# Kernel optimization log

Hardware: AMD Instinct MI355X
Metric: run time of the kernel (lower is better)

## Reference

```python
import jax, jax.numpy as jnp
import numpy as np

RADIUS = 1.5
PARTITION_NUM = 5
OUT_CHANNEL = 128
IN_CHANNEL = 64
EPS = 1e-5


def setup_inputs() -> dict:
    key = jax.random.key(0)
    ks = jax.random.split(key, 10)
    B, N, npoint, K = 16, 8192, 2048, 32
    D = 61  # points feature dim; in_channel = D + 3 = 64
    xyz = jax.random.normal(ks[0], (B, N, 3), dtype=jnp.float32)
    points = jax.random.normal(ks[1], (B, N, D), dtype=jnp.float32)
    local_coordinates = jax.random.uniform(ks[2], (B, npoint, K, 3), dtype=jnp.float32)
    neighbor_lists = jax.random.randint(ks[3], (B, npoint, K), 0, N)
    data_idx = jax.random.randint(ks[4], (B, npoint), 0, N)
    parameter_list = jnp.zeros((1,), dtype=jnp.float32)
    # params (torch Linear stored transposed here: [in, out])
    W1 = jax.random.normal(ks[5], (IN_CHANNEL * PARTITION_NUM, OUT_CHANNEL), dtype=jnp.float32) * 0.02
    b1 = jnp.zeros((OUT_CHANNEL,), dtype=jnp.float32)
    g1 = jnp.ones((OUT_CHANNEL,), dtype=jnp.float32)
    be1 = jnp.zeros((OUT_CHANNEL,), dtype=jnp.float32)
    W2 = jax.random.normal(ks[6], (OUT_CHANNEL, OUT_CHANNEL), dtype=jnp.float32) * 0.02
    b2 = jnp.zeros((OUT_CHANNEL,), dtype=jnp.float32)
    g2 = jnp.ones((OUT_CHANNEL,), dtype=jnp.float32)
    be2 = jnp.zeros((OUT_CHANNEL,), dtype=jnp.float32)
    return dict(xyz=xyz, points=points, local_coordinates=local_coordinates,
                neighbor_lists=neighbor_lists, parameter_list=parameter_list,
                data_idx=data_idx, W1=W1, b1=b1, g1=g1, be1=be1,
                W2=W2, b2=b2, g2=g2, be2=be2)


def _forward(xyz, points, local_coordinates, parameter_list,
             W1, b1, g1, be1, W2, b2, g2, be2, neighbor_lists, data_idx):
    B, N, _ = xyz.shape
    _, npoint, K = neighbor_lists.shape
    # new_xyz = index_points(xyz, data_idx)
    new_xyz = jnp.take_along_axis(xyz, data_idx[:, :, None], axis=1)  # [B, npoint, 3]
    # points = cat(points, xyz) -> in_channel features
    pts = jnp.concatenate([points, xyz], axis=2)  # [B, N, C]
    C = pts.shape[-1]
    # gather neighbor feats: [B, npoint, K, C] (permute chain in torch is a net identity)
    idx = neighbor_lists.reshape(B, npoint * K)
    grouped = jnp.take_along_axis(pts, idx[:, :, None], axis=1).reshape(B, npoint, K, C)
    # circle_conv: radial binning + scatter-add over partition bins
    lc = local_coordinates.reshape(B, npoint, K, 3)
    dist = jnp.linalg.norm(lc[..., 0:2], axis=-1)          # [B, npoint, K]
    dist = jnp.minimum(dist / RADIUS, 0.99)                # cut(x, 0.99)
    bins = jnp.floor(dist * PARTITION_NUM).astype(jnp.int32)
    onehot = jax.nn.one_hot(bins, PARTITION_NUM, dtype=grouped.dtype)  # [B, npoint, K, P]
    feature = jnp.einsum('bnkp,bnkc->bnpc', onehot, grouped)           # scatter_add
    feature = feature.reshape(B * npoint, PARTITION_NUM * C)
    # Linear + BatchNorm1d (training-mode batch stats) + ReLU
    x = feature @ W1 + b1                                  # [B*npoint, out]
    mu = x.mean(axis=0)
    var = x.var(axis=0)
    x = jax.nn.relu(g1 * (x - mu) / jnp.sqrt(var + EPS) + be1)
    x = x.reshape(B, npoint, -1)
    # Linear + BatchNorm1d over channels + ReLU
    y = x @ W2 + b2                                        # [B, npoint, out]
    mu2 = y.mean(axis=(0, 1))
    var2 = y.var(axis=(0, 1))
    new_points = jax.nn.relu(g2 * (y - mu2) / jnp.sqrt(var2 + EPS) + be2)
    return new_xyz, new_points


def reference(xyz, points, local_coordinates, neighbor_lists, parameter_list,
              data_idx, W1, b1, g1, be1, W2, b2, g2, be2):
    return _forward(xyz, points, local_coordinates, parameter_list,
                    W1, b1, g1, be1, W2, b2, g2, be2, neighbor_lists, data_idx)
```

## Files before the change

### kernel.cpp

```cpp
#include <hip/hip_runtime.h>
#include <hip/hip_bf16.h>
#include <math.h>

#define B_SZ     16
#define N_PTS    8192
#define NPOINT   2048
#define KNBR     32
#define D_FEAT   61
#define C_IN     64
#define P_BINS   5
#define C_OUT    128
#define M_ROWS   (B_SZ * NPOINT)
#define K1       (C_IN * P_BINS)
#define EPSV     1e-5f

typedef __attribute__((ext_vector_type(8))) short bf16x8;
typedef __attribute__((ext_vector_type(4))) float f32x4;

__device__ __forceinline__ unsigned short f2bf_rne(float v) {
    unsigned u = __float_as_uint(v);
    u += 0x7fffu + ((u >> 16) & 1u);
    return (unsigned short)(u >> 16);
}
__device__ __forceinline__ float bf2f(unsigned short v) {
    return __uint_as_float(((unsigned)v) << 16);
}

__device__ __forceinline__ size_t fragB_idx(int n, int c) {
    return ((size_t)((c >> 5) * 8 + (n >> 4)) << 9) +
           ((((c >> 3) & 3) * 16 + (n & 15)) << 3) + (c & 7);
}

__global__ __launch_bounds__(256) void prep_kernel(
    const float* __restrict__ W1, const float* __restrict__ W2,
    unsigned short* __restrict__ W1f, unsigned short* __restrict__ W2f,
    float* __restrict__ st)
{
    const int gid = blockIdx.x * 256 + threadIdx.x;
    if (gid < 40960) {
        int c = gid >> 7, n = gid & 127;
        W1f[fragB_idx(n, c)] = f2bf_rne(W1[gid]);
    } else if (gid < 57344) {
        int i = gid - 40960;
        int c = i >> 7, n = i & 127;
        W2f[fragB_idx(n, c)] = f2bf_rne(W2[i]);
    } else if (gid < 61440) {
        st[gid - 57344] = 0.f;
    }
}

__global__ __launch_bounds__(256) void fusedg1_kernel(
    const float* __restrict__ xyz, const float* __restrict__ points,
    const float* __restrict__ lc, const int* __restrict__ nl,
    const int* __restrict__ didx, const unsigned short* __restrict__ W1f,
    const float* __restrict__ b1, unsigned short* __restrict__ x1f,
    float* __restrict__ st, float* __restrict__ newxyz)
{
    const int g    = blockIdx.x;
    const int xcd  = g & 7;
    const int slot = g >> 3;
    const int b    = 2 * xcd + (slot >> 7);
    const int t16  = slot & 127;
    const int tile = b * 128 + t16;
    const int wave = threadIdx.x >> 6;
    const int lane = threadIdx.x & 63;
    const int k    = lane & 31;
    const int lm   = lane & 15, kg = lane >> 4;
    const int kgl  = (lane >> 3) & 3, jl = lane & 7, khalf = lane >> 5;

    __shared__ int s_srt[4][32];
    __shared__ __align__(16) unsigned short sA[10 * 512];

    const float* __restrict__ pbase = points + (size_t)b * N_PTS * D_FEAT;
    const float* __restrict__ xbase = xyz + (size_t)b * N_PTS * 3;

    for (int p = 0; p < 4; ++p) {
        const int mloc = wave * 4 + p;
        const int bid  = tile * 16 + mloc;
        const size_t nbase = (size_t)bid * KNBR;

        const float x = lc[(nbase + k) * 3 + 0];
        const float y = lc[(nbase + k) * 3 + 1];
        const float dd = fminf(sqrtf(x * x + y * y) * (1.0f / 1.5f), 0.99f);
        int bin = (int)(dd * 5.0f);
        bin = bin > 4 ? 4 : (bin < 0 ? 0 : bin);
        const int n = nl[nbase + k];

        unsigned m0 = (unsigned)__ballot(bin == 0);
        unsigned m1 = (unsigned)__ballot(bin == 1);
        unsigned m2 = (unsigned)__ballot(bin == 2);
        unsigned m3 = (unsigned)__ballot(bin == 3);
        unsigned m4 = (unsigned)__ballot(bin == 4);
        const int c0n = __popc(m0), c1n = __popc(m1);
        const int c2n = __popc(m2), c3n = __popc(m3);
        const int e0 = c0n, e1 = e0 + c1n, e2 = e1 + c2n, e3 = e2 + c3n;

        int start = (bin > 0 ? c0n : 0) + (bin > 1 ? c1n : 0) +
                    (bin > 2 ? c2n : 0) + (bin > 3 ? c3n : 0);
        unsigned mymask = m0;
        mymask = bin == 1 ? m1 : mymask;
        mymask = bin == 2 ? m2 : mymask;
        mymask = bin == 3 ? m3 : mymask;
        mymask = bin == 4 ? m4 : mymask;
        const int pos = start + __popc(mymask & ((1u << k) - 1u));

        if (lane < 32) s_srt[wave][pos] = n;
        if (lane >= 32 && lane < 35) {
            const int di = didx[bid];
            newxyz[(size_t)bid * 3 + (lane - 32)] = xbase[(size_t)di * 3 + (lane - 32)];
        }

        float v[32];
        #pragma unroll
        for (int kk = 0; kk < 32; ++kk) {
            const int nr = __builtin_amdgcn_readfirstlane(s_srt[wave][kk]);
            float t;
            if (lane < D_FEAT) t = pbase[nr * D_FEAT + lane];
            else               t = xbase[nr * 3 + (lane - D_FEAT)];
            v[kk] = t;
        }

        float acc = 0.f, pre0 = 0.f, pre1 = 0.f, pre2 = 0.f, pre3 = 0.f;
        #pragma unroll
        for (int kk = 0; kk < 32; ++kk) {
            acc += v[kk];
            const int kp = kk + 1;
            if (kp == e0) pre0 = acc;
            if (kp == e1) pre1 = acc;
            if (kp == e2) pre2 = acc;
            if (kp == e3) pre3 = acc;
        }
        float vals[5];
        vals[0] = pre0;
        vals[1] = pre1 - pre0;
        vals[2] = pre2 - pre1;
        vals[3] = pre3 - pre2;
        vals[4] = acc - pre3;

        #pragma unroll
        for (int bb = 0; bb < 5; ++bb) {
            const int kb = bb * 2 + khalf;
            sA[kb * 512 + (kgl * 16 + mloc) * 8 + jl] = f2bf_rne(vals[bb]);
        }
    }
    __syncthreads();

    f32x4 acc0 = {}, acc1 = {};
    #pragma unroll
    for (int kb = 0; kb < 10; ++kb) {
        bf16x8 a = *(const bf16x8*)&sA[kb * 512 + lane * 8];
        bf16x8 w0 = *(const bf16x8*)(W1f + ((size_t)(kb * 8 + wave * 2) << 9) + lane * 8);
        bf16x8 w1 = *(const bf16x8*)(W1f + ((size_t)(kb * 8 + wave * 2 + 1) << 9) + lane * 8);
        acc0 = __builtin_amdgcn_mfma_f32_16x16x32_bf16(a, w0, acc0, 0, 0, 0);
        acc1 = __builtin_amdgcn_mfma_f32_16x16x32_bf16(a, w1, acc1, 0, 0, 0);
    }

    const int rep = (g & 7) * 128;
    #pragma unroll
    for (int q = 0; q < 2; ++q) {
        const f32x4 A = q ? acc1 : acc0;
        const int col = (wave * 2 + q) * 16 + lm;
        const float bb = b1[col];
        float ls = 0.f, lq = 0.f;
        #pragma unroll
        for (int i = 0; i < 4; ++i) {
            float vv = A[i] + bb;
            const size_t idx = (((size_t)(tile * 4 + (col >> 5))) << 9) +
                               ((((col >> 3) & 3) * 16 + kg * 4 + i) << 3) + (col & 7);
            x1f[idx] = f2bf_rne(vv);
            ls += vv; lq += vv * vv;
        }
        ls += __shfl_xor(ls, 16); ls += __shfl_xor(ls, 32);
        lq += __shfl_xor(lq, 16); lq += __shfl_xor(lq, 32);
        if (kg == 0) {
            atomicAdd(&st[rep + col], ls);
            atomicAdd(&st[1024 + rep + col], lq);
        }
    }
}

__global__ __launch_bounds__(256) void gemm2_mfma(
    const unsigned short* __restrict__ Xf,
    const float* __restrict__ st_in,
    const float* __restrict__ g1, const float* __restrict__ be1,
    const unsigned short* __restrict__ Wf, const float* __restrict__ bias,
    unsigned short* __restrict__ out, float* __restrict__ st)
{
    __shared__ float sc[128], sh[128];
    __shared__ float s_s[4][128], s_q[4][128];
    const int tid = threadIdx.x;
    if (tid < 128) {
        float s = 0.f, q = 0.f;
        #pragma unroll
        for (int r = 0; r < 8; ++r) {
            s += st_in[r * 128 + tid];
            q += st_in[1024 + r * 128 + tid];
        }
        float mu  = s * (1.0f / (float)M_ROWS);
        float var = q * (1.0f / (float)M_ROWS) - mu * mu;
        float iv  = 1.0f / sqrtf(var + EPSV);
        float sg  = g1[tid] * iv;
        sc[tid] = sg;
        sh[tid] = be1[tid] - mu * sg;
    }
    __syncthreads();

    const int g    = blockIdx.x;
    const int xcd  = g & 7;
    const int slot = g >> 3;
    const int bb_  = 2 * xcd + (slot >> 5);
    const int tile = (bb_ * 32 + (slot & 31)) * 4 + (tid >> 6);

    const int wave = tid >> 6, lane = tid & 63;
    const int lm = lane & 15, kg = lane >> 4;

    f32x4 acc[8] = {};
    #pragma unroll
    for (int kb = 0; kb < 4; ++kb) {
        const int c0 = kb * 32 + kg * 8;
        bf16x8 xr = *(const bf16x8*)(Xf + (((size_t)(tile * 4 + kb)) << 9) + lane * 8);
        f32x4 s0 = *(const f32x4*)&sc[c0];
        f32x4 s1 = *(const f32x4*)&sc[c0 + 4];
        f32x4 h0 = *(const f32x4*)&sh[c0];
        f32x4 h1 = *(const f32x4*)&sh[c0 + 4];
        bf16x8 a;
        #pragma unroll
        for (int j = 0; j < 4; ++j) {
            a[j]     = (short)f2bf_rne(fmaxf(0.f, s0[j] * bf2f((unsigned short)xr[j]) + h0[j]));
            a[4 + j] = (short)f2bf_rne(fmaxf(0.f, s1[j] * bf2f((unsigned short)xr[4 + j]) + h1[j]));
        }
        #pragma unroll
        for (int nf = 0; nf < 8; ++nf) {
            bf16x8 bfr = *(const bf16x8*)(Wf + (((size_t)(kb * 8 + nf)) << 9) + lane * 8);
            acc[nf] = __builtin_amdgcn_mfma_f32_16x16x32_bf16(a, bfr, acc[nf], 0, 0, 0);
        }
    }

    const int orow = tile * 16 + kg * 4;
    #pragma unroll
    for (int nf = 0; nf < 8; ++nf) {
        const int col = nf * 16 + lm;
        const float bb = bias[col];
        float ls = 0.f, lq = 0.f;
        #pragma unroll
        for (int i = 0; i < 4; ++i) {
            float v = acc[nf][i] + bb;
            out[(size_t)(orow + i) * C_OUT + col] = f2bf_rne(v);
            ls += v; lq += v * v;
        }
        ls += __shfl_xor(ls, 16); ls += __shfl_xor(ls, 32);
        lq += __shfl_xor(lq, 16); lq += __shfl_xor(lq, 32);
        if (kg == 0) { s_s[wave][col] = ls; s_q[wave][col] = lq; }
    }
    __syncthreads();
    if (tid < 128) {
        const int rep = (g & 7) * 128;
        float ts = s_s[0][tid] + s_s[1][tid] + s_s[2][tid] + s_s[3][tid];
        float tq = s_q[0][tid] + s_q[1][tid] + s_q[2][tid] + s_q[3][tid];
        atomicAdd(&st[2048 + rep + tid], ts);
        atomicAdd(&st[3072 + rep + tid], tq);
    }
}

__global__ __launch_bounds__(256) void out_kernel(
    const unsigned short* __restrict__ Y, const float* __restrict__ st,
    const float* __restrict__ g2, const float* __restrict__ be2,
    float* __restrict__ out)
{
    __shared__ float sc[128], sh[128];
    const int tid = threadIdx.x;
    if (tid < 128) {
        float s = 0.f, q = 0.f;
        #pragma unroll
        for (int r = 0; r < 8; ++r) {
            s += st[2048 + r * 128 + tid];
            q += st[3072 + r * 128 + tid];
        }
        float mu  = s * (1.0f / (float)M_ROWS);
        float var = q * (1.0f / (float)M_ROWS) - mu * mu;
        float iv  = 1.0f / sqrtf(var + EPSV);
        float sg  = g2[tid] * iv;
        sc[tid] = sg;
        sh[tid] = be2[tid] - mu * sg;
    }
    __syncthreads();

    const size_t e8 = (size_t)blockIdx.x * 256 + tid;
    bf16x8 v = ((const bf16x8*)Y)[e8];
    const int cb = (int)((e8 * 8) & 127);
    float4 r0, r1;
    r0.x = fmaxf(0.f, sc[cb + 0] * bf2f((unsigned short)v[0]) + sh[cb + 0]);
    r0.y = fmaxf(0.f, sc[cb + 1] * bf2f((unsigned short)v[1]) + sh[cb + 1]);
    r0.z = fmaxf(0.f, sc[cb + 2] * bf2f((unsigned short)v[2]) + sh[cb + 2]);
    r0.w = fmaxf(0.f, sc[cb + 3] * bf2f((unsigned short)v[3]) + sh[cb + 3]);
    r1.x = fmaxf(0.f, sc[cb + 4] * bf2f((unsigned short)v[4]) + sh[cb + 4]);
    r1.y = fmaxf(0.f, sc[cb + 5] * bf2f((unsigned short)v[5]) + sh[cb + 5]);
    r1.z = fmaxf(0.f, sc[cb + 6] * bf2f((unsigned short)v[6]) + sh[cb + 6]);
    r1.w = fmaxf(0.f, sc[cb + 7] * bf2f((unsigned short)v[7]) + sh[cb + 7]);
    ((float4*)out)[e8 * 2]     = r0;
    ((float4*)out)[e8 * 2 + 1] = r1;
}

extern "C" void kernel_launch(void* const* d_in, const int* in_sizes, int n_in,
                              void* d_out, int out_size, void* d_ws, size_t ws_size,
                              hipStream_t stream)
{
    const float* xyz    = (const float*)d_in[0];
    const float* points = (const float*)d_in[1];
    const float* lc     = (const float*)d_in[2];
    const int*   nl     = (const int*)d_in[3];
    const int*   didx   = (const int*)d_in[5];
    const float* W1     = (const float*)d_in[6];
    const float* b1     = (const float*)d_in[7];
    const float* g1     = (const float*)d_in[8];
    const float* be1    = (const float*)d_in[9];
    const float* W2     = (const float*)d_in[10];
    const float* b2     = (const float*)d_in[11];
    const float* g2     = (const float*)d_in[12];
    const float* be2    = (const float*)d_in[13];

    float* out = (float*)d_out;
    char*  ws  = (char*)d_ws;

    unsigned short* x1f = (unsigned short*)ws;
    unsigned short* yb  = (unsigned short*)(ws + 8388608);
    unsigned short* W1f = (unsigned short*)(ws + 16777216);
    unsigned short* W2f = (unsigned short*)(ws + 16859136);
    float*          st  = (float*)(ws + 16891904);

    prep_kernel<<<240, 256, 0, stream>>>(W1, W2, W1f, W2f, st);
    fusedg1_kernel<<<M_ROWS / 16, 256, 0, stream>>>(xyz, points, lc, nl, didx,
                                                    W1f, b1, x1f, st, out);
    gemm2_mfma<<<M_ROWS / 64, 256, 0, stream>>>(x1f, st, g1, be1,
                                                W2f, b2, yb, st);
    out_kernel<<<(M_ROWS * C_OUT) / (256 * 8), 256, 0, stream>>>(
        yb, st, g2, be2, out + (size_t)M_ROWS * 3);
}
```

Measured before the change: 168.4 us.

## Pre-pack point features to bf16 rows and retile gemm2 with wider stat replicas

A new prep pass converts points+xyz into a padded bf16 [B*N,64] table, so the neighbor gather in the fused first GEMM reads aligned 128-byte rows instead of fp32 61-wide rows plus a separate xyz lookup. Binning is done as direct per-bin accumulation rather than prefix sums. gemm2 switches to 16-row tiles with column-split waves and more blocks, and the BatchNorm statistic replicas grow from 8 to 16 to reduce atomic contention. The extra conversion pass reads and writes the full point table, which adds memory traffic, and bf16 inputs reduce precision before summation.

```diff
diff --git a/kernel.cpp b/kernel.cpp
--- a/kernel.cpp
+++ b/kernel.cpp
@@ -13,6 +13,7 @@
 #define M_ROWS   (B_SZ * NPOINT)
 #define K1       (C_IN * P_BINS)
 #define EPSV     1e-5f
+#define NREP     16
 
 typedef __attribute__((ext_vector_type(8))) short bf16x8;
 typedef __attribute__((ext_vector_type(4))) float f32x4;
@@ -32,25 +33,41 @@
 }
 
 __global__ __launch_bounds__(256) void prep_kernel(
+    const float* __restrict__ points, const float* __restrict__ xyz,
     const float* __restrict__ W1, const float* __restrict__ W2,
-    unsigned short* __restrict__ W1f, unsigned short* __restrict__ W2f,
-    float* __restrict__ st)
-{
-    const int gid = blockIdx.x * 256 + threadIdx.x;
-    if (gid < 40960) {
-        int c = gid >> 7, n = gid & 127;
-        W1f[fragB_idx(n, c)] = f2bf_rne(W1[gid]);
-    } else if (gid < 57344) {
-        int i = gid - 40960;
-        int c = i >> 7, n = i & 127;
-        W2f[fragB_idx(n, c)] = f2bf_rne(W2[i]);
-    } else if (gid < 61440) {
-        st[gid - 57344] = 0.f;
+    unsigned short* __restrict__ ptsb, unsigned short* __restrict__ W1f,
+    unsigned short* __restrict__ W2f, float* __restrict__ st)
+{
+    const int blk = blockIdx.x;
+    const int tid = threadIdx.x;
+    if (blk < 32768) {
+        const int xcd  = blk & 7;
+        const int slot = blk >> 3;
+        const int b    = 2 * xcd + (slot >> 11);
+        const int rin  = (slot & 2047) * 4 + (tid >> 6);
+        const int row  = b * N_PTS + rin;
+        const int c    = tid & 63;
+        float v;
+        if (c < D_FEAT) v = points[(size_t)row * D_FEAT + c];
+        else            v = xyz[(size_t)row * 3 + (c - D_FEAT)];
+        ptsb[((size_t)row << 6) | c] = f2bf_rne(v);
+    } else {
+        const int gid = (blk - 32768) * 256 + tid;
+        if (gid < 40960) {
+            int c = gid >> 7, n = gid & 127;
+            W1f[fragB_idx(n, c)] = f2bf_rne(W1[gid]);
+        } else if (gid < 57344) {
+            int i = gid - 40960;
+            int c = i >> 7, n = i & 127;
+            W2f[fragB_idx(n, c)] = f2bf_rne(W2[i]);
+        } else {
+            st[gid - 57344] = 0.f;
+        }
     }
 }
 
 __global__ __launch_bounds__(256) void fusedg1_kernel(
-    const float* __restrict__ xyz, const float* __restrict__ points,
+    const unsigned short* __restrict__ ptsb, const float* __restrict__ xyz,
     const float* __restrict__ lc, const int* __restrict__ nl,
     const int* __restrict__ didx, const unsigned short* __restrict__ W1f,
     const float* __restrict__ b1, unsigned short* __restrict__ x1f,
@@ -60,8 +77,7 @@
     const int xcd  = g & 7;
     const int slot = g >> 3;
     const int b    = 2 * xcd + (slot >> 7);
-    const int t16  = slot & 127;
-    const int tile = b * 128 + t16;
+    const int tile = b * 128 + (slot & 127);
     const int wave = threadIdx.x >> 6;
     const int lane = threadIdx.x & 63;
     const int k    = lane & 31;
@@ -71,7 +87,7 @@
     __shared__ int s_srt[4][32];
     __shared__ __align__(16) unsigned short sA[10 * 512];
 
-    const float* __restrict__ pbase = points + (size_t)b * N_PTS * D_FEAT;
+    const unsigned short* __restrict__ tb = ptsb + (((size_t)b * N_PTS) << 6);
     const float* __restrict__ xbase = xyz + (size_t)b * N_PTS * 3;
 
     for (int p = 0; p < 4; ++p) {
@@ -110,33 +126,27 @@
             newxyz[(size_t)bid * 3 + (lane - 32)] = xbase[(size_t)di * 3 + (lane - 32)];
         }
 
-        float v[32];
+        const int srtv = s_srt[wave][k];
+
+        unsigned short vv[32];
         #pragma unroll
         for (int kk = 0; kk < 32; ++kk) {
-            const int nr = __builtin_amdgcn_readfirstlane(s_srt[wave][kk]);
-            float t;
-            if (lane < D_FEAT) t = pbase[nr * D_FEAT + lane];
-            else               t = xbase[nr * 3 + (lane - D_FEAT)];
-            v[kk] = t;
-        }
-
-        float acc = 0.f, pre0 = 0.f, pre1 = 0.f, pre2 = 0.f, pre3 = 0.f;
+            const int nr = __builtin_amdgcn_readlane(srtv, kk);
+            vv[kk] = tb[((size_t)nr << 6) | lane];
+        }
+
+        float a0 = 0.f, a1 = 0.f, a2 = 0.f, a3 = 0.f, a4 = 0.f;
         #pragma unroll
         for (int kk = 0; kk < 32; ++kk) {
-            acc += v[kk];
-            const int kp = kk + 1;
-            if (kp == e0) pre0 = acc;
-            if (kp == e1) pre1 = acc;
-            if (kp == e2) pre2 = acc;
-            if (kp == e3) pre3 = acc;
-        }
-        float vals[5];
-        vals[0] = pre0;
-        vals[1] = pre1 - pre0;
-        vals[2] = pre2 - pre1;
-        vals[3] = pre3 - pre2;
-        vals[4] = acc - pre3;
-
+            const float v = bf2f(vv[kk]);
+            if      (kk < e0) a0 += v;
+            else if (kk < e1) a1 += v;
+            else if (kk < e2) a2 += v;
+            else if (kk < e3) a3 += v;
+            else              a4 += v;
+        }
+
+        const float vals[5] = {a0, a1, a2, a3, a4};
         #pragma unroll
         for (int bb = 0; bb < 5; ++bb) {
             const int kb = bb * 2 + khalf;
@@ -155,7 +165,7 @@
         acc1 = __builtin_amdgcn_mfma_f32_16x16x32_bf16(a, w1, acc1, 0, 0, 0);
     }
 
-    const int rep = (g & 7) * 128;
+    const int rep = (g & (NREP - 1)) * 128;
     #pragma unroll
     for (int q = 0; q < 2; ++q) {
         const f32x4 A = q ? acc1 : acc0;
@@ -164,17 +174,17 @@
         float ls = 0.f, lq = 0.f;
         #pragma unroll
         for (int i = 0; i < 4; ++i) {
-            float vv = A[i] + bb;
+            float vv2 = A[i] + bb;
             const size_t idx = (((size_t)(tile * 4 + (col >> 5))) << 9) +
                                ((((col >> 3) & 3) * 16 + kg * 4 + i) << 3) + (col & 7);
-            x1f[idx] = f2bf_rne(vv);
-            ls += vv; lq += vv * vv;
+            x1f[idx] = f2bf_rne(vv2);
+            ls += vv2; lq += vv2 * vv2;
         }
         ls += __shfl_xor(ls, 16); ls += __shfl_xor(ls, 32);
         lq += __shfl_xor(lq, 16); lq += __shfl_xor(lq, 32);
         if (kg == 0) {
             atomicAdd(&st[rep + col], ls);
-            atomicAdd(&st[1024 + rep + col], lq);
+            atomicAdd(&st[2048 + rep + col], lq);
         }
     }
 }
@@ -187,14 +197,13 @@
     unsigned short* __restrict__ out, float* __restrict__ st)
 {
     __shared__ float sc[128], sh[128];
-    __shared__ float s_s[4][128], s_q[4][128];
     const int tid = threadIdx.x;
     if (tid < 128) {
         float s = 0.f, q = 0.f;
         #pragma unroll
-        for (int r = 0; r < 8; ++r) {
+        for (int r = 0; r < NREP; ++r) {
             s += st_in[r * 128 + tid];
-            q += st_in[1024 + r * 128 + tid];
+            q += st_in[2048 + r * 128 + tid];
         }
         float mu  = s * (1.0f / (float)M_ROWS);
         float var = q * (1.0f / (float)M_ROWS) - mu * mu;
@@ -208,57 +217,49 @@
     const int g    = blockIdx.x;
     const int xcd  = g & 7;
     const int slot = g >> 3;
-    const int bb_  = 2 * xcd + (slot >> 5);
-    const int tile = (bb_ * 32 + (slot & 31)) * 4 + (tid >> 6);
+    const int b    = 2 * xcd + (slot >> 7);
+    const int tile = b * 128 + (slot & 127);
 
     const int wave = tid >> 6, lane = tid & 63;
     const int lm = lane & 15, kg = lane >> 4;
 
-    f32x4 acc[8] = {};
+    f32x4 acc0 = {}, acc1 = {};
     #pragma unroll
     for (int kb = 0; kb < 4; ++kb) {
         const int c0 = kb * 32 + kg * 8;
         bf16x8 xr = *(const bf16x8*)(Xf + (((size_t)(tile * 4 + kb)) << 9) + lane * 8);
-        f32x4 s0 = *(const f32x4*)&sc[c0];
-        f32x4 s1 = *(const f32x4*)&sc[c0 + 4];
-        f32x4 h0 = *(const f32x4*)&sh[c0];
-        f32x4 h1 = *(const f32x4*)&sh[c0 + 4];
         bf16x8 a;
         #pragma unroll
-        for (int j = 0; j < 4; ++j) {
-            a[j]     = (short)f2bf_rne(fmaxf(0.f, s0[j] * bf2f((unsigned short)xr[j]) + h0[j]));
-            a[4 + j] = (short)f2bf_rne(fmaxf(0.f, s1[j] * bf2f((unsigned short)xr[4 + j]) + h1[j]));
-        }
-        #pragma unroll
-        for (int nf = 0; nf < 8; ++nf) {
-            bf16x8 bfr = *(const bf16x8*)(Wf + (((size_t)(kb * 8 + nf)) << 9) + lane * 8);
-            acc[nf] = __builtin_amdgcn_mfma_f32_16x16x32_bf16(a, bfr, acc[nf], 0, 0, 0);
-        }
+        for (int j = 0; j < 8; ++j) {
+            float xv = bf2f((unsigned short)xr[j]);
+            a[j] = (short)f2bf_rne(fmaxf(0.f, sc[c0 + j] * xv + sh[c0 + j]));
+        }
+        bf16x8 w0 = *(const bf16x8*)(Wf + ((size_t)(kb * 8 + wave * 2) << 9) + lane * 8);
+        bf16x8 w1 = *(const bf16x8*)(Wf + ((size_t)(kb * 8 + wave * 2 + 1) << 9) + lane * 8);
+        acc0 = __builtin_amdgcn_mfma_f32_16x16x32_bf16(a, w0, acc0, 0, 0, 0);
+        acc1 = __builtin_amdgcn_mfma_f32_16x16x32_bf16(a, w1, acc1, 0, 0, 0);
     }
 
     const int orow = tile * 16 + kg * 4;
+    const int rep = (g & (NREP - 1)) * 128;
     #pragma unroll
-    for (int nf = 0; nf < 8; ++nf) {
-        const int col = nf * 16 + lm;
+    for (int q = 0; q < 2; ++q) {
+        const f32x4 A = q ? acc1 : acc0;
+        const int col = (wave * 2 + q) * 16 + lm;
         const float bb = bias[col];
         float ls = 0.f, lq = 0.f;
         #pragma unroll
         for (int i = 0; i < 4; ++i) {
-            float v = acc[nf][i] + bb;
+            float v = A[i] + bb;
             out[(size_t)(orow + i) * C_OUT + col] = f2bf_rne(v);
             ls += v; lq += v * v;
         }
         ls += __shfl_xor(ls, 16); ls += __shfl_xor(ls, 32);
         lq += __shfl_xor(lq, 16); lq += __shfl_xor(lq, 32);
-        if (kg == 0) { s_s[wave][col] = ls; s_q[wave][col] = lq; }
-    }
-    __syncthreads();
-    if (tid < 128) {
-        const int rep = (g & 7) * 128;
-        float ts = s_s[0][tid] + s_s[1][tid] + s_s[2][tid] + s_s[3][tid];
-        float tq = s_q[0][tid] + s_q[1][tid] + s_q[2][tid] + s_q[3][tid];
-        atomicAdd(&st[2048 + rep + tid], ts);
-        atomicAdd(&st[3072 + rep + tid], tq);
+        if (kg == 0) {
+            atomicAdd(&st[4096 + rep + col], ls);
+            atomicAdd(&st[6144 + rep + col], lq);
+        }
     }
 }
 
@@ -272,9 +273,9 @@
     if (tid < 128) {
         float s = 0.f, q = 0.f;
         #pragma unroll
-        for (int r = 0; r < 8; ++r) {
-            s += st[2048 + r * 128 + tid];
-            q += st[3072 + r * 128 + tid];
+        for (int r = 0; r < NREP; ++r) {
+            s += st[4096 + r * 128 + tid];
+            q += st[6144 + r * 128 + tid];
         }
         float mu  = s * (1.0f / (float)M_ROWS);
         float var = q * (1.0f / (float)M_ROWS) - mu * mu;
@@ -322,16 +323,18 @@
     float* out = (float*)d_out;
     char*  ws  = (char*)d_ws;
 
-    unsigned short* x1f = (unsigned short*)ws;
-    unsigned short* yb  = (unsigned short*)(ws + 8388608);
-    unsigned short* W1f = (unsigned short*)(ws + 16777216);
-    unsigned short* W2f = (unsigned short*)(ws + 16859136);
-    float*          st  = (float*)(ws + 16891904);
-
-    prep_kernel<<<240, 256, 0, stream>>>(W1, W2, W1f, W2f, st);
-    fusedg1_kernel<<<M_ROWS / 16, 256, 0, stream>>>(xyz, points, lc, nl, didx,
+    unsigned short* ptsb = (unsigned short*)ws;
+    unsigned short* x1f  = (unsigned short*)(ws + 16777216);
+    unsigned short* yb   = (unsigned short*)(ws + 25165824);
+    unsigned short* W1f  = (unsigned short*)(ws + 33554432);
+    unsigned short* W2f  = (unsigned short*)(ws + 33636352);
+    float*          st   = (float*)(ws + 33669120);
+
+    prep_kernel<<<32768 + 256, 256, 0, stream>>>(points, xyz, W1, W2,
+                                                 ptsb, W1f, W2f, st);
+    fusedg1_kernel<<<M_ROWS / 16, 256, 0, stream>>>(ptsb, xyz, lc, nl, didx,
                                                     W1f, b1, x1f, st, out);
-    gemm2_mfma<<<M_ROWS / 64, 256, 0, stream>>>(x1f, st, g1, be1,
+    gemm2_mfma<<<M_ROWS / 16, 256, 0, stream>>>(x1f, st, g1, be1,
                                                 W2f, b2, yb, st);
     out_kernel<<<(M_ROWS * C_OUT) / (256 * 8), 256, 0, stream>>>(
         yb, st, g2, be2, out + (size_t)M_ROWS * 3);
```

New measurement: 188.1 us. 1.12x slower.
